# Kernel optimization log

Hardware: AMD Instinct MI355X
Metric: run time of the kernel (lower is better)

The kernel has to match this reference:

```python
import jax, jax.numpy as jnp
import numpy as np

B, N, E, FIN, H, D = 256, 1024, 8192, 8, 4, 5
HD = H * D            # GATv2: 4 heads * 5 dim, concat -> 20
OBS = N               # flattened obs length
AOUT = 64             # action_space_output_dim (aggregator output)
HID = 256             # hidden_size
NOUT = 64             # num_outputs (logits)
NEG = 0.2             # GATv2 leaky_relu negative slope
EPS = 1e-5            # batchnorm eps


def setup_inputs() -> dict:
    key = jax.random.key(0)
    ks = jax.random.split(key, 16)
    def lin(k, i, o):
        return (jax.random.normal(k, (i, o), jnp.float32) / np.sqrt(i)).astype(jnp.float32)
    return {
        "x": jax.random.normal(ks[0], (B, N, FIN), jnp.float32),
        "obs": jax.random.normal(ks[1], (B, OBS), jnp.float32),
        "edge_index": jax.random.randint(ks[2], (2, E), 0, N),
        # GATv2 layer 0 (in=FIN) and layer 1 (in=HD)
        "Wl0": lin(ks[3], FIN, HD), "Wr0": lin(ks[4], FIN, HD),
        "att0": (jax.random.normal(ks[5], (H, D), jnp.float32) * 0.1), "b0": jnp.zeros((HD,), jnp.float32),
        "Wl1": lin(ks[6], HD, HD), "Wr1": lin(ks[7], HD, HD),
        "att1": (jax.random.normal(ks[8], (H, D), jnp.float32) * 0.1), "b1": jnp.zeros((HD,), jnp.float32),
        # BatchNorm params per layer (over feature dim)
        "g0": jnp.ones((HD,), jnp.float32), "be0": jnp.zeros((HD,), jnp.float32),
        "g1": jnp.ones((HD,), jnp.float32), "be1": jnp.zeros((HD,), jnp.float32),
        # aggregator linear (mean pool -> action-space dim)
        "Wagg": lin(ks[9], HD, AOUT), "bagg": jnp.zeros((AOUT,), jnp.float32),
        # logits MLP: cat(agg, obs) -> HID -> HID//2 -> NOUT (tanh activations)
        "W1": lin(ks[10], AOUT + OBS, HID), "bh1": jnp.zeros((HID,), jnp.float32),
        "W2": lin(ks[11], HID, HID // 2), "bh2": jnp.zeros((HID // 2,), jnp.float32),
        "Wout": lin(ks[12], HID // 2, NOUT), "bout": jnp.zeros((NOUT,), jnp.float32),
    }


def _gatv2_single(x, src, dst, Wl, Wr, att, bias):
    # x: [N, Fin]; src/dst: [Es] (with self loops)
    xl = (x @ Wl).reshape(N, H, D)
    xr = (x @ Wr).reshape(N, H, D)
    m = jax.nn.leaky_relu(xl[src] + xr[dst], NEG)        # [Es, H, D]
    e = jnp.einsum('ehd,hd->eh', m, att)                 # [Es, H]
    emax = jax.ops.segment_max(e, dst, num_segments=N)   # every node has a self loop
    p = jnp.exp(e - emax[dst])
    s = jax.ops.segment_sum(p, dst, num_segments=N)
    alpha = p / s[dst]                                   # softmax over incoming edges
    out = jax.ops.segment_sum(alpha[:, :, None] * xl[src], dst, num_segments=N)
    return out.reshape(N, HD) + bias


def _bn(x, g, b):
    # training-mode batchnorm over all (batch, node) positions, per feature
    mu = x.mean(axis=(0, 1))
    var = x.var(axis=(0, 1))
    return (x - mu) * jax.lax.rsqrt(var + EPS) * g + b


def reference(x, obs, edge_index, Wl0, Wr0, att0, b0, Wl1, Wr1, att1, b1,
              g0, be0, g1, be1, Wagg, bagg, W1, bh1, W2, bh2, Wout, bout):
    loops = jnp.arange(N)
    src = jnp.concatenate([edge_index[0], loops])
    dst = jnp.concatenate([edge_index[1], loops])
    layer = lambda xb, Wl, Wr, att, bias: jax.vmap(
        lambda xn: _gatv2_single(xn, src, dst, Wl, Wr, att, bias))(xb)
    h = layer(x, Wl0, Wr0, att0, b0)       # [B, N, HD]
    h = _bn(h, g0, be0)
    h = layer(h, Wl1, Wr1, att1, b1)
    h = _bn(h, g1, be1)
    agg = h.mean(axis=1) @ Wagg + bagg     # mean graph pooling -> [B, AOUT]
    f = jnp.concatenate([agg, obs], axis=1)
    f = jnp.tanh(f @ W1 + bh1)
    f = jnp.tanh(f @ W2 + bh2)
    return f @ Wout + bout                 # logits [B, NOUT]
```

## Files before the change

kernel.cpp:

```cpp
#include <hip/hip_runtime.h>
#include <hip/hip_bf16.h>
#include <math.h>

typedef unsigned short u16;
typedef __attribute__((ext_vector_type(8))) short short8;
typedef __attribute__((ext_vector_type(4))) float floatx4;

constexpr int kN   = 1024;
constexpr int kB   = 256;
constexpr int kE   = 8192;
constexpr int kHD  = 20;
constexpr float kEps = 1e-5f;

static __device__ __forceinline__ float u16_bf16_to_f32(u16 v) {
  return __uint_as_float(((unsigned)v) << 16);
}
static __device__ __forceinline__ void unpack2(unsigned u, float& a, float& b) {
  a = __uint_as_float(u << 16);
  b = __uint_as_float(u & 0xffff0000u);
}
static __device__ __forceinline__ u16 f2bf(float f) {
  __hip_bfloat16 h = __float2bfloat16(f);
  return *reinterpret_cast<u16*>(&h);
}
static __device__ __forceinline__ unsigned pack_bf16(float a, float b) {
  return (unsigned)f2bf(a) | ((unsigned)f2bf(b) << 16);
}

static __device__ __forceinline__ int detect_flag(const unsigned* __restrict__ x) {
  __shared__ int sflag;
  int t = threadIdx.x;
  if (t < 64) {
    unsigned w = x[t];
    unsigned e = (w >> 7) & 0xFFu;
    unsigned long long bl = __ballot(e >= 114u && e <= 136u);
    if (t == 0) sflag = (__popcll(bl) >= 32) ? 1 : 0;
  }
  __syncthreads();
  return sflag;
}

static __device__ __forceinline__ size_t gidx(int n, int b) {
  return ((size_t)(b >> 6) * kN + n) * 64 + (b & 63);
}

struct SmallConv {
  const void* src[17];
  float* dst[17];
  int n[17];
};

struct PrepArgs {
  const unsigned* x;
  const int* ei;
  const void* W1; const void* W2; const void* Wout;
  SmallConv sc;
  u16* xb;
  u16* W1p; u16* W2p; u16* Woutp;
  int* csr_off; int* csr_src;
  float* sums;
};

static __device__ __forceinline__ void repack_one(const void* src, u16* dst, int c, int N, int srcbf) {
  int n = c % N;
  int t2 = c / N;
  int q = t2 & 3, kb = t2 >> 2;
  int k0 = kb * 32 + q * 8;
  u16 w[8];
  if (srcbf) {
    const u16* s = (const u16*)src;
#pragma unroll
    for (int j = 0; j < 8; j++) w[j] = s[(size_t)(k0 + j) * N + n];
  } else {
    const float* s = (const float*)src;
#pragma unroll
    for (int j = 0; j < 8; j++) w[j] = f2bf(s[(size_t)(k0 + j) * N + n]);
  }
  uint4 out;
  out.x = (unsigned)w[0] | ((unsigned)w[1] << 16);
  out.y = (unsigned)w[2] | ((unsigned)w[3] << 16);
  out.z = (unsigned)w[4] | ((unsigned)w[5] << 16);
  out.w = (unsigned)w[6] | ((unsigned)w[7] << 16);
  *((uint4*)(dst + (size_t)c * 8)) = out;
}

__global__ __launch_bounds__(256) void prep_kernel(PrepArgs pa) {
  int bid = blockIdx.x;
  int t = threadIdx.x;
  if (bid == 0) {
    __shared__ int cnt[kN];
    __shared__ int cur[kN];
    __shared__ int wsum[4];
    for (int i = t; i < kN; i += 256) cnt[i] = 0;
    __syncthreads();
    for (int e = t; e < kE; e += 256) atomicAdd(&cnt[pa.ei[kE + e]], 1);
    __syncthreads();
    int d[4], pre[4];
    int s = 0;
#pragma unroll
    for (int j = 0; j < 4; j++) { d[j] = cnt[t * 4 + j] + 1; pre[j] = s; s += d[j]; }
    int lane = t & 63;
    int v = s;
    for (int o = 1; o < 64; o <<= 1) { int u = __shfl_up(v, o); if (lane >= o) v += u; }
    if (lane == 63) wsum[t >> 6] = v;
    __syncthreads();
    int wbase = 0;
    for (int w = 0; w < (t >> 6); w++) wbase += wsum[w];
    int base = wbase + v - s;
#pragma unroll
    for (int j = 0; j < 4; j++) {
      pa.csr_off[t * 4 + j] = base + pre[j];
      cur[t * 4 + j] = base + pre[j];
    }
    if (t == 255) pa.csr_off[kN] = wbase + v;
    __syncthreads();
    for (int e = t; e < kE; e += 256) {
      int sv = pa.ei[e], dv = pa.ei[kE + e];
      int pos = atomicAdd(&cur[dv], 1);
      pa.csr_src[pos] = sv;
    }
    for (int i = t; i < kN; i += 256) {
      int pos = atomicAdd(&cur[i], 1);
      pa.csr_src[pos] = i;
    }
    return;
  }
  int flag = detect_flag(pa.x);
  if (bid == 1) {
    for (int i = t; i < 640; i += 256) pa.sums[i] = 0.f;
    for (int k = 0; k < 17; k++) {
      int n = pa.sc.n[k];
      float* d = pa.sc.dst[k];
      if (flag) {
        const u16* s = (const u16*)pa.sc.src[k];
        for (int i = t; i < n; i += 256) d[i] = u16_bf16_to_f32(s[i]);
      } else {
        const float* s = (const float*)pa.sc.src[k];
        for (int i = t; i < n; i += 256) d[i] = s[i];
      }
    }
    return;
  }
  if (bid < 158) {
    int c = (bid - 2) * 256 + t;
    if (c < 34816) repack_one(pa.W1, pa.W1p, c, 256, flag);
    else if (c < 34816 + 4096) repack_one(pa.W2, pa.W2p, c - 34816, 128, flag);
    else if (c < 34816 + 4096 + 1024) repack_one(pa.Wout, pa.Woutp, c - 34816 - 4096, 64, flag);
    return;
  }
  int rid = (bid - 158) * 256 + t;
  int b = rid >> 10, n = rid & 1023;
  uint4 o;
  if (flag) {
    o = *((const uint4*)((const u16*)pa.x + (size_t)rid * 8));
  } else {
    const float4* s = (const float4*)((const float*)pa.x + (size_t)rid * 8);
    float4 r0 = s[0], r1 = s[1];
    o.x = pack_bf16(r0.x, r0.y); o.y = pack_bf16(r0.z, r0.w);
    o.z = pack_bf16(r1.x, r1.y); o.w = pack_bf16(r1.z, r1.w);
  }
  *((uint4*)(pa.xb + ((size_t)n * kB + b) * 8)) = o;
}

__global__ __launch_bounds__(256) void lin0_kernel(const u16* __restrict__ xb,
                                                   const float* __restrict__ Wl,
                                                   u16* __restrict__ xlb) {
  __shared__ float wl[160];
  int t = threadIdx.x;
  if (t < 160) wl[t] = Wl[t];
  __syncthreads();
  int n = blockIdx.x, b = t;
  uint4 r = *((const uint4*)(xb + ((size_t)n * kB + b) * 8));
  float xi[8];
  unpack2(r.x, xi[0], xi[1]); unpack2(r.y, xi[2], xi[3]);
  unpack2(r.z, xi[4], xi[5]); unpack2(r.w, xi[6], xi[7]);
  float ol[kHD];
#pragma unroll
  for (int f = 0; f < kHD; f++) {
    float al = 0.f;
#pragma unroll
    for (int i = 0; i < 8; i++) al = fmaf(xi[i], wl[i * kHD + f], al);
    ol[f] = al;
  }
  uint2* pl = (uint2*)(xlb + gidx(n, b) * kHD);
#pragma unroll
  for (int k = 0; k < 5; k++)
    pl[k] = make_uint2(pack_bf16(ol[4 * k], ol[4 * k + 1]), pack_bf16(ol[4 * k + 2], ol[4 * k + 3]));
}

__global__ __launch_bounds__(256) void lin1_kernel(const u16* __restrict__ hb,
                                                   const float* __restrict__ sums0,
                                                   const float* __restrict__ g0,
                                                   const float* __restrict__ be0,
                                                   const float* __restrict__ Wl1,
                                                   u16* __restrict__ xlb) {
  __shared__ float wl[400], sbl[kHD], afold[kHD], cfold[kHD], tot[2 * kHD];
  int t = threadIdx.x;
  if (t < 2 * kHD) {
    float v = 0.f;
    for (int k = 0; k < 8; k++) v += sums0[k * 2 * kHD + t];
    tot[t] = v;
  }
  __syncthreads();
  if (t < kHD) {
    const float inv = 1.0f / (float)(kN * kB);
    float mu = tot[t] * inv;
    float var = tot[kHD + t] * inv - mu * mu;
    float a = g0[t] * rsqrtf(var + kEps);
    afold[t] = a;
    cfold[t] = be0[t] - mu * a;
  }
  __syncthreads();
  for (int idx = t; idx < 400; idx += 256) wl[idx] = afold[idx / kHD] * Wl1[idx];
  if (t < kHD) {
    float s = 0.f;
    for (int f = 0; f < kHD; f++) s += cfold[f] * Wl1[f * kHD + t];
    sbl[t] = s;
  }
  __syncthreads();
  int n = blockIdx.x, b = t;
  float hv[kHD];
  {
    const uint2* p = (const uint2*)(hb + gidx(n, b) * kHD);
#pragma unroll
    for (int k = 0; k < 5; k++) {
      uint2 v = p[k];
      unpack2(v.x, hv[4 * k], hv[4 * k + 1]);
      unpack2(v.y, hv[4 * k + 2], hv[4 * k + 3]);
    }
  }
  float ol[kHD];
#pragma unroll
  for (int j = 0; j < kHD; j++) {
    float al = sbl[j];
#pragma unroll
    for (int f = 0; f < kHD; f++) al = fmaf(hv[f], wl[f * kHD + j], al);
    ol[j] = al;
  }
  uint2* pl = (uint2*)(xlb + gidx(n, b) * kHD);
#pragma unroll
  for (int k = 0; k < 5; k++)
    pl[k] = make_uint2(pack_bf16(ol[4 * k], ol[4 * k + 1]), pack_bf16(ol[4 * k + 2], ol[4 * k + 3]));
}

__global__ __launch_bounds__(64) void attn0_kernel(const u16* __restrict__ xlb,
                                                   const u16* __restrict__ xb,
                                                   const float* __restrict__ Wr0,
                                                   const float* __restrict__ att,
                                                   const float* __restrict__ bias,
                                                   const int* __restrict__ csr_off,
                                                   const int* __restrict__ csr_src,
                                                   u16* __restrict__ hout,
                                                   float* __restrict__ sums) {
  __shared__ float satt[kHD], sbias[kHD], swr[160];
  __shared__ int ssrc[128];
  __shared__ float red[2 * kHD];
  int t = threadIdx.x;
  int tb = blockIdx.x & 3;
  int n = blockIdx.x >> 2;
  if (t < kHD) { satt[t] = att[t]; sbias[t] = bias[t]; }
  for (int i = t; i < 160; i += 64) swr[i] = Wr0[i];
  int beg = csr_off[n], end = csr_off[n + 1];
  int deg = end - beg;
  for (int i = t; i < deg && i < 128; i += 64) ssrc[i] = csr_src[beg + i];
  __syncthreads();
  int b = (tb << 6) | t;
  float xrv[kHD];
  {
    uint4 r = *((const uint4*)(xb + ((size_t)n * kB + b) * 8));
    float xi[8];
    unpack2(r.x, xi[0], xi[1]); unpack2(r.y, xi[2], xi[3]);
    unpack2(r.z, xi[4], xi[5]); unpack2(r.w, xi[6], xi[7]);
#pragma unroll
    for (int f = 0; f < kHD; f++) {
      float a = 0.f;
#pragma unroll
      for (int i = 0; i < 8; i++) a = fmaf(xi[i], swr[i * kHD + f], a);
      xrv[f] = a;
    }
  }
  float s[4] = {0.f, 0.f, 0.f, 0.f};
  float acc[kHD];
#pragma unroll
  for (int f = 0; f < kHD; f++) acc[f] = 0.f;

  const size_t tilebase = (size_t)tb * kN * 64 * kHD;
  auto loadrow = [&](int i, uint2 (&rr)[5]) {
    int srcn = (i < 128) ? ssrc[i] : csr_src[beg + i];
    const uint2* p = (const uint2*)(xlb + tilebase + ((size_t)srcn * 64 + t) * kHD);
#pragma unroll
    for (int k = 0; k < 5; k++) rr[k] = p[k];
  };
  auto consume = [&](uint2 (&rr)[5]) {
    float xs[kHD];
#pragma unroll
    for (int k = 0; k < 5; k++) {
      unpack2(rr[k].x, xs[4 * k], xs[4 * k + 1]);
      unpack2(rr[k].y, xs[4 * k + 2], xs[4 * k + 3]);
    }
#pragma unroll
    for (int hh = 0; hh < 4; hh++) {
      float e = 0.f;
#pragma unroll
      for (int d2 = 0; d2 < 5; d2++) {
        int f = hh * 5 + d2;
        float v = xs[f] + xrv[f];
        v = fmaxf(v, 0.2f * v);
        e = fmaf(v, satt[f], e);
      }
      float p = __expf(e);
      s[hh] += p;
#pragma unroll
      for (int d2 = 0; d2 < 5; d2++) {
        int f = hh * 5 + d2;
        acc[f] = fmaf(p, xs[f], acc[f]);
      }
    }
  };

  uint2 r0[5], r1[5];
  loadrow(0, r0);
  if (deg > 1) loadrow(1, r1);
  int i = 0;
  for (; i + 1 < deg; i += 2) {
    consume(r0);
    if (i + 2 < deg) loadrow(i + 2, r0);
    consume(r1);
    if (i + 3 < deg) loadrow(i + 3, r1);
  }
  if (i < deg) consume(r0);

  float hv[kHD];
#pragma unroll
  for (int hh = 0; hh < 4; hh++) {
    float inv = 1.f / s[hh];
#pragma unroll
    for (int d2 = 0; d2 < 5; d2++) {
      int f = hh * 5 + d2;
      hv[f] = fmaf(acc[f], inv, sbias[f]);
    }
  }
  {
    uint2* ph = (uint2*)(hout + tilebase + ((size_t)n * 64 + t) * kHD);
#pragma unroll
    for (int k = 0; k < 5; k++)
      ph[k] = make_uint2(pack_bf16(hv[4 * k], hv[4 * k + 1]), pack_bf16(hv[4 * k + 2], hv[4 * k + 3]));
  }
#pragma unroll
  for (int f = 0; f < kHD; f++) {
    float a = hv[f], q = hv[f] * hv[f];
    for (int o = 32; o > 0; o >>= 1) { a += __shfl_down(a, o); q += __shfl_down(q, o); }
    if (t == 0) { red[f] = a; red[kHD + f] = q; }
  }
  __syncthreads();
  if (t < 2 * kHD) atomicAdd(&sums[(blockIdx.x & 7) * 2 * kHD + t], red[t]);
}

__global__ __launch_bounds__(64) void attn1_kernel(const u16* __restrict__ xlb,
                                                   const u16* __restrict__ hb,
                                                   const float* __restrict__ sums0,
                                                   const float* __restrict__ g0,
                                                   const float* __restrict__ be0,
                                                   const float* __restrict__ Wr1,
                                                   const float* __restrict__ att,
                                                   const float* __restrict__ bias,
                                                   const int* __restrict__ csr_off,
                                                   const int* __restrict__ csr_src,
                                                   u16* __restrict__ hout) {
  __shared__ float satt[kHD], sbias[kHD], swr[400], sbr[kHD];
  __shared__ float afold[kHD], cfold[kHD], tot[2 * kHD];
  __shared__ int ssrc[128];
  int t = threadIdx.x;
  int tb = blockIdx.x & 3;
  int n = blockIdx.x >> 2;
  if (t < kHD) { satt[t] = att[t]; sbias[t] = bias[t]; }
  if (t < 2 * kHD) {
    float v = 0.f;
    for (int k = 0; k < 8; k++) v += sums0[k * 2 * kHD + t];
    tot[t] = v;
  }
  int beg = csr_off[n], end = csr_off[n + 1];
  int deg = end - beg;
  for (int i = t; i < deg && i < 128; i += 64) ssrc[i] = csr_src[beg + i];
  __syncthreads();
  if (t < kHD) {
    const float inv = 1.0f / (float)(kN * kB);
    float mu = tot[t] * inv;
    float var = tot[kHD + t] * inv - mu * mu;
    float a = g0[t] * rsqrtf(var + kEps);
    afold[t] = a;
    cfold[t] = be0[t] - mu * a;
  }
  __syncthreads();
  for (int idx = t; idx < 400; idx += 64) swr[idx] = afold[idx / kHD] * Wr1[idx];
  if (t < kHD) {
    float sv = 0.f;
    for (int f = 0; f < kHD; f++) sv = fmaf(cfold[f], Wr1[f * kHD + t], sv);
    sbr[t] = sv;
  }
  __syncthreads();
  const size_t tilebase = (size_t)tb * kN * 64 * kHD;
  float xrv[kHD];
  {
    float hv0[kHD];
    const uint2* p = (const uint2*)(hb + tilebase + ((size_t)n * 64 + t) * kHD);
#pragma unroll
    for (int k = 0; k < 5; k++) {
      uint2 v = p[k];
      unpack2(v.x, hv0[4 * k], hv0[4 * k + 1]);
      unpack2(v.y, hv0[4 * k + 2], hv0[4 * k + 3]);
    }
#pragma unroll
    for (int j = 0; j < kHD; j++) {
      float a = sbr[j];
#pragma unroll
      for (int f = 0; f < kHD; f++) a = fmaf(hv0[f], swr[f * kHD + j], a);
      xrv[j] = a;
    }
  }
  float s[4] = {0.f, 0.f, 0.f, 0.f};
  float acc[kHD];
#pragma unroll
  for (int f = 0; f < kHD; f++) acc[f] = 0.f;

  auto loadrow = [&](int i, uint2 (&rr)[5]) {
    int srcn = (i < 128) ? ssrc[i] : csr_src[beg + i];
    const uint2* p = (const uint2*)(xlb + tilebase + ((size_t)srcn * 64 + t) * kHD);
#pragma unroll
    for (int k = 0; k < 5; k++) rr[k] = p[k];
  };
  auto consume = [&](uint2 (&rr)[5]) {
    float xs[kHD];
#pragma unroll
    for (int k = 0; k < 5; k++) {
      unpack2(rr[k].x, xs[4 * k], xs[4 * k + 1]);
      unpack2(rr[k].y, xs[4 * k + 2], xs[4 * k + 3]);
    }
#pragma unroll
    for (int hh = 0; hh < 4; hh++) {
      float e = 0.f;
#pragma unroll
      for (int d2 = 0; d2 < 5; d2++) {
        int f = hh * 5 + d2;
        float v = xs[f] + xrv[f];
        v = fmaxf(v, 0.2f * v);
        e = fmaf(v, satt[f], e);
      }
      float p = __expf(e);
      s[hh] += p;
#pragma unroll
      for (int d2 = 0; d2 < 5; d2++) {
        int f = hh * 5 + d2;
        acc[f] = fmaf(p, xs[f], acc[f]);
      }
    }
  };

  uint2 r0[5], r1[5];
  loadrow(0, r0);
  if (deg > 1) loadrow(1, r1);
  int i = 0;
  for (; i + 1 < deg; i += 2) {
    consume(r0);
    if (i + 2 < deg) loadrow(i + 2, r0);
    consume(r1);
    if (i + 3 < deg) loadrow(i + 3, r1);
  }
  if (i < deg) consume(r0);

  float hv[kHD];
#pragma unroll
  for (int hh = 0; hh < 4; hh++) {
    float inv = 1.f / s[hh];
#pragma unroll
    for (int d2 = 0; d2 < 5; d2++) {
      int f = hh * 5 + d2;
      hv[f] = fmaf(acc[f], inv, sbias[f]);
    }
  }
  uint2* ph = (uint2*)(hout + tilebase + ((size_t)n * 64 + t) * kHD);
#pragma unroll
  for (int k = 0; k < 5; k++)
    ph[k] = make_uint2(pack_bf16(hv[4 * k], hv[4 * k + 1]), pack_bf16(hv[4 * k + 2], hv[4 * k + 3]));
}

__global__ __launch_bounds__(64) void pool_kernel(const u16* __restrict__ hb2,
                                                  float* __restrict__ pool_part,
                                                  float* __restrict__ sums1) {
  __shared__ float red[2 * kHD];
  int t = threadIdx.x;
  int tb = blockIdx.x & 3;
  int ch = blockIdx.x >> 2;
  const size_t tilebase = (size_t)tb * kN * 64 * kHD;
  float acc[kHD], q[kHD];
#pragma unroll
  for (int f = 0; f < kHD; f++) { acc[f] = 0.f; q[f] = 0.f; }
  for (int j = 0; j < 64; j++) {
    int n = ch * 64 + j;
    const uint2* p = (const uint2*)(hb2 + tilebase + ((size_t)n * 64 + t) * kHD);
#pragma unroll
    for (int k = 0; k < 5; k++) {
      uint2 v = p[k];
      float a0, a1, a2, a3;
      unpack2(v.x, a0, a1); unpack2(v.y, a2, a3);
      acc[4 * k] += a0;     q[4 * k] += a0 * a0;
      acc[4 * k + 1] += a1; q[4 * k + 1] += a1 * a1;
      acc[4 * k + 2] += a2; q[4 * k + 2] += a2 * a2;
      acc[4 * k + 3] += a3; q[4 * k + 3] += a3 * a3;
    }
  }
  int b = tb * 64 + t;
  float4* pp = (float4*)(pool_part + ((size_t)ch * kB + b) * kHD);
#pragma unroll
  for (int k = 0; k < 5; k++)
    pp[k] = make_float4(acc[4 * k], acc[4 * k + 1], acc[4 * k + 2], acc[4 * k + 3]);
#pragma unroll
  for (int f = 0; f < kHD; f++) {
    float a = acc[f], qq = q[f];
    for (int o = 32; o > 0; o >>= 1) { a += __shfl_down(a, o); qq += __shfl_down(qq, o); }
    if (t == 0) { red[f] = a; red[kHD + f] = qq; }
  }
  __syncthreads();
  if (t < 2 * kHD) atomicAdd(&sums1[(blockIdx.x & 7) * 2 * kHD + t], red[t]);
}

__global__ __launch_bounds__(256) void mlp_kernel(const float* __restrict__ pool_part,
                                                  const float* __restrict__ sums1,
                                                  const float* __restrict__ g1,
                                                  const float* __restrict__ be1,
                                                  const float* __restrict__ Wagg,
                                                  const float* __restrict__ bagg,
                                                  const void* __restrict__ obsraw,
                                                  const u16* __restrict__ W1p,
                                                  const u16* __restrict__ W2p,
                                                  const u16* __restrict__ Woutp,
                                                  const float* __restrict__ bh1,
                                                  const float* __restrict__ bh2,
                                                  const float* __restrict__ bout,
                                                  const unsigned* __restrict__ xdet,
                                                  void* __restrict__ outv) {
  __shared__ __align__(16) u16 fins[16][1096];
  __shared__ __align__(16) u16 h1s[16][264];
  __shared__ __align__(16) u16 h2s[16][136];
  __shared__ float sWagg[1280], pv[16][kHD], a1[kHD], c1[kHD], tot[2 * kHD];
  int flag = detect_flag(xdet);
  int t = threadIdx.x;
  int m0 = blockIdx.x * 16;
  if (t < 2 * kHD) {
    float v = 0.f;
    for (int k = 0; k < 8; k++) v += sums1[k * 2 * kHD + t];
    tot[t] = v;
  }
  for (int idx = t; idx < 1280; idx += 256) sWagg[idx] = Wagg[idx];
  __syncthreads();
  if (t < kHD) {
    const float inv = 1.0f / (float)(kN * kB);
    float mu = tot[t] * inv;
    float var = tot[kHD + t] * inv - mu * mu;
    float a = g1[t] * rsqrtf(var + kEps);
    a1[t] = a;
    c1[t] = be1[t] - mu * a;
  }
  __syncthreads();
  for (int idx = t; idx < 16 * kHD; idx += 256) {
    int bl = idx / kHD, f = idx % kHD;
    float p = 0.f;
    for (int ch = 0; ch < 16; ch++) p += pool_part[((size_t)ch * kB + m0 + bl) * kHD + f];
    pv[bl][f] = (p * (1.0f / kN)) * a1[f] + c1[f];
  }
  for (int idx = t * 8; idx < 16 * 1024; idx += 2048) {
    int r = idx >> 10, c = idx & 1023;
    uint4 o;
    if (flag) {
      o = *((const uint4*)((const u16*)obsraw + (size_t)(m0 + r) * 1024 + c));
    } else {
      const float4* sp = (const float4*)((const float*)obsraw + (size_t)(m0 + r) * 1024 + c);
      float4 r0 = sp[0], r1 = sp[1];
      o.x = pack_bf16(r0.x, r0.y); o.y = pack_bf16(r0.z, r0.w);
      o.z = pack_bf16(r1.x, r1.y); o.w = pack_bf16(r1.z, r1.w);
    }
    *(uint4*)&fins[r][64 + c] = o;
  }
  __syncthreads();
  {
    int j = t & 63, rg = t >> 6;
    for (int r = rg; r < 16; r += 4) {
      float a = bagg[j];
#pragma unroll
      for (int f = 0; f < kHD; f++) a = fmaf(pv[r][f], sWagg[f * 64 + j], a);
      fins[r][j] = f2bf(a);
    }
  }
  __syncthreads();
  int wave = t >> 6, lane = t & 63, lo = lane & 15, quad = lane >> 4;
  {
    floatx4 acc[4] = {{0.f, 0.f, 0.f, 0.f}, {0.f, 0.f, 0.f, 0.f}, {0.f, 0.f, 0.f, 0.f}, {0.f, 0.f, 0.f, 0.f}};
    for (int kb = 0; kb < 34; kb++) {
      short8 a = *(const short8*)&fins[lo][kb * 32 + quad * 8];
#pragma unroll
      for (int nt = 0; nt < 4; nt++) {
        int n0 = (wave * 4 + nt) * 16;
        short8 bf = *(const short8*)(W1p + ((size_t)(kb * 4 + quad) * 256 + n0 + lo) * 8);
        acc[nt] = __builtin_amdgcn_mfma_f32_16x16x32_bf16(a, bf, acc[nt], 0, 0, 0);
      }
    }
#pragma unroll
    for (int nt = 0; nt < 4; nt++) {
      int n0 = (wave * 4 + nt) * 16;
      float bias = bh1[n0 + lo];
#pragma unroll
      for (int r = 0; r < 4; r++) h1s[quad * 4 + r][n0 + lo] = f2bf(tanhf(acc[nt][r] + bias));
    }
  }
  __syncthreads();
  {
    floatx4 acc[2] = {{0.f, 0.f, 0.f, 0.f}, {0.f, 0.f, 0.f, 0.f}};
    for (int kb = 0; kb < 8; kb++) {
      short8 a = *(const short8*)&h1s[lo][kb * 32 + quad * 8];
#pragma unroll
      for (int nt = 0; nt < 2; nt++) {
        int n0 = (wave * 2 + nt) * 16;
        short8 bf = *(const short8*)(W2p + ((size_t)(kb * 4 + quad) * 128 + n0 + lo) * 8);
        acc[nt] = __builtin_amdgcn_mfma_f32_16x16x32_bf16(a, bf, acc[nt], 0, 0, 0);
      }
    }
#pragma unroll
    for (int nt = 0; nt < 2; nt++) {
      int n0 = (wave * 2 + nt) * 16;
      float bias = bh2[n0 + lo];
#pragma unroll
      for (int r = 0; r < 4; r++) h2s[quad * 4 + r][n0 + lo] = f2bf(tanhf(acc[nt][r] + bias));
    }
  }
  __syncthreads();
  {
    int n0 = wave * 16;
    floatx4 acc = {0.f, 0.f, 0.f, 0.f};
    for (int kb = 0; kb < 4; kb++) {
      short8 a = *(const short8*)&h2s[lo][kb * 32 + quad * 8];
      short8 bf = *(const short8*)(Woutp + ((size_t)(kb * 4 + quad) * 64 + n0 + lo) * 8);
      acc = __builtin_amdgcn_mfma_f32_16x16x32_bf16(a, bf, acc, 0, 0, 0);
    }
    float bias = bout[n0 + lo];
    if (flag) {
      __hip_bfloat16* o = (__hip_bfloat16*)outv;
#pragma unroll
      for (int r = 0; r < 4; r++)
        o[(size_t)(m0 + quad * 4 + r) * 64 + n0 + lo] = __float2bfloat16(acc[r] + bias);
    } else {
      float* o = (float*)outv;
#pragma unroll
      for (int r = 0; r < 4; r++)
        o[(size_t)(m0 + quad * 4 + r) * 64 + n0 + lo] = acc[r] + bias;
    }
  }
}

extern "C" void kernel_launch(void* const* d_in, const int* in_sizes, int n_in,
                              void* d_out, int out_size, void* d_ws, size_t ws_size,
                              hipStream_t stream) {
  const int* ei = (const int*)d_in[2];
  char* ws = (char*)d_ws;

  float* sums0     = (float*)(ws + 0);
  float* sums1     = (float*)(ws + 1280);
  int*   csr_off   = (int*)(ws + 2816);
  int*   csr_src   = (int*)(ws + 7168);
  float* convf     = (float*)(ws + 44288);
  u16*   W1p       = (u16*)(ws + 56832);
  u16*   W2p       = (u16*)(ws + 613888);
  u16*   Woutp     = (u16*)(ws + 679424);
  float* pool_part = (float*)(ws + 695808);
  u16*   xb        = (u16*)(ws + 1023744);
  u16*   xlb       = (u16*)(ws + 5218048);
  u16*   hb        = (u16*)(ws + 15703808);
  u16*   hb2       = (u16*)(ws + 26189568);

  const int s_din[17] = {3, 4, 5, 6, 7, 8, 9, 10, 11, 12, 13, 14, 15, 16, 18, 20, 22};
  const int s_n[17]   = {160, 160, 20, 20, 400, 400, 20, 20, 20, 20, 20, 20, 1280, 64, 256, 128, 64};
  SmallConv sc;
  float* fptr[17];
  {
    size_t co = 0;
    for (int i = 0; i < 17; i++) {
      sc.src[i] = d_in[s_din[i]];
      sc.dst[i] = convf + co;
      sc.n[i] = s_n[i];
      fptr[i] = convf + co;
      co += (size_t)s_n[i];
    }
  }
  float* Wl0_f = fptr[0],  *Wr0_f = fptr[1],  *att0_f = fptr[2], *b0_f = fptr[3];
  float* Wl1_f = fptr[4],  *Wr1_f = fptr[5],  *att1_f = fptr[6], *b1_f = fptr[7];
  float* g0_f = fptr[8],   *be0_f = fptr[9],  *g1_f = fptr[10],  *be1_f = fptr[11];
  float* Wagg_f = fptr[12], *bagg_f = fptr[13], *bh1_f = fptr[14], *bh2_f = fptr[15];
  float* bout_f = fptr[16];

  PrepArgs pa;
  pa.x = (const unsigned*)d_in[0];
  pa.ei = ei;
  pa.W1 = d_in[17]; pa.W2 = d_in[19]; pa.Wout = d_in[21];
  pa.sc = sc;
  pa.xb = xb;
  pa.W1p = W1p; pa.W2p = W2p; pa.Woutp = Woutp;
  pa.csr_off = csr_off; pa.csr_src = csr_src;
  pa.sums = sums0;

  prep_kernel<<<1182, 256, 0, stream>>>(pa);
  lin0_kernel<<<kN, 256, 0, stream>>>(xb, Wl0_f, xlb);
  attn0_kernel<<<4 * kN, 64, 0, stream>>>(xlb, xb, Wr0_f, att0_f, b0_f, csr_off, csr_src, hb, sums0);
  lin1_kernel<<<kN, 256, 0, stream>>>(hb, sums0, g0_f, be0_f, Wl1_f, xlb);
  attn1_kernel<<<4 * kN, 64, 0, stream>>>(xlb, hb, sums0, g0_f, be0_f, Wr1_f, att1_f, b1_f,
                                          csr_off, csr_src, hb2);
  pool_kernel<<<64, 64, 0, stream>>>(hb2, pool_part, sums1);
  mlp_kernel<<<16, 256, 0, stream>>>(pool_part, sums1, g1_f, be1_f, Wagg_f, bagg_f, d_in[1],
                                     W1p, W2p, Woutp, bh1_f, bh2_f, bout_f,
                                     (const unsigned*)d_in[0], d_out);
}
```

Baseline: 260.5 us.

## Fuse each GATv2 layer into one per-graph block with LDS-resident features

New measurement: 493.2 us. 1.89x slower.

```diff
diff --git a/kernel.cpp b/kernel.cpp
--- a/kernel.cpp
+++ b/kernel.cpp
@@ -40,10 +40,6 @@
   return sflag;
 }
 
-static __device__ __forceinline__ size_t gidx(int n, int b) {
-  return ((size_t)(b >> 6) * kN + n) * 64 + (b & 63);
-}
-
 struct SmallConv {
   const void* src[17];
   float* dst[17];
@@ -55,7 +51,6 @@
   const int* ei;
   const void* W1; const void* W2; const void* Wout;
   SmallConv sc;
-  u16* xb;
   u16* W1p; u16* W2p; u16* Woutp;
   int* csr_off; int* csr_src;
   float* sums;
@@ -141,66 +136,149 @@
     }
     return;
   }
-  if (bid < 158) {
-    int c = (bid - 2) * 256 + t;
-    if (c < 34816) repack_one(pa.W1, pa.W1p, c, 256, flag);
-    else if (c < 34816 + 4096) repack_one(pa.W2, pa.W2p, c - 34816, 128, flag);
-    else if (c < 34816 + 4096 + 1024) repack_one(pa.Wout, pa.Woutp, c - 34816 - 4096, 64, flag);
-    return;
-  }
-  int rid = (bid - 158) * 256 + t;
-  int b = rid >> 10, n = rid & 1023;
-  uint4 o;
+  int c = (bid - 2) * 256 + t;
+  if (c < 34816) repack_one(pa.W1, pa.W1p, c, 256, flag);
+  else if (c < 34816 + 4096) repack_one(pa.W2, pa.W2p, c - 34816, 128, flag);
+  else if (c < 34816 + 4096 + 1024) repack_one(pa.Wout, pa.Woutp, c - 34816 - 4096, 64, flag);
+}
+
+__global__ __launch_bounds__(1024) void gnn0_kernel(const unsigned* __restrict__ xraw,
+                                                    const float* __restrict__ Wl0,
+                                                    const float* __restrict__ Wr0,
+                                                    const float* __restrict__ att0,
+                                                    const float* __restrict__ b0,
+                                                    const int* __restrict__ csr_off,
+                                                    const int* __restrict__ csr_src,
+                                                    u16* __restrict__ h,
+                                                    float* __restrict__ sums0) {
+  __shared__ u16 sxl[kN * kHD];
+  __shared__ float swl[160], swr[160], satt[kHD], sbias[kHD];
+  __shared__ float red[16][2 * kHD];
+  int flag = detect_flag(xraw);
+  int t = threadIdx.x, b = blockIdx.x;
+  if (t < 160) { swl[t] = Wl0[t]; swr[t] = Wr0[t]; }
+  else if (t >= 256 && t < 256 + kHD) satt[t - 256] = att0[t - 256];
+  else if (t >= 512 && t < 512 + kHD) sbias[t - 512] = b0[t - 512];
+  __syncthreads();
+  float xi[8];
   if (flag) {
-    o = *((const uint4*)((const u16*)pa.x + (size_t)rid * 8));
+    uint4 r = *((const uint4*)((const u16*)xraw + ((size_t)b * kN + t) * 8));
+    unpack2(r.x, xi[0], xi[1]); unpack2(r.y, xi[2], xi[3]);
+    unpack2(r.z, xi[4], xi[5]); unpack2(r.w, xi[6], xi[7]);
   } else {
-    const float4* s = (const float4*)((const float*)pa.x + (size_t)rid * 8);
-    float4 r0 = s[0], r1 = s[1];
-    o.x = pack_bf16(r0.x, r0.y); o.y = pack_bf16(r0.z, r0.w);
-    o.z = pack_bf16(r1.x, r1.y); o.w = pack_bf16(r1.z, r1.w);
-  }
-  *((uint4*)(pa.xb + ((size_t)n * kB + b) * 8)) = o;
-}
-
-__global__ __launch_bounds__(256) void lin0_kernel(const u16* __restrict__ xb,
-                                                   const float* __restrict__ Wl,
-                                                   u16* __restrict__ xlb) {
-  __shared__ float wl[160];
-  int t = threadIdx.x;
-  if (t < 160) wl[t] = Wl[t];
-  __syncthreads();
-  int n = blockIdx.x, b = t;
-  uint4 r = *((const uint4*)(xb + ((size_t)n * kB + b) * 8));
-  float xi[8];
-  unpack2(r.x, xi[0], xi[1]); unpack2(r.y, xi[2], xi[3]);
-  unpack2(r.z, xi[4], xi[5]); unpack2(r.w, xi[6], xi[7]);
-  float ol[kHD];
+    const float4* s4 = (const float4*)((const float*)xraw + ((size_t)b * kN + t) * 8);
+    float4 r0 = s4[0], r1 = s4[1];
+    xi[0] = r0.x; xi[1] = r0.y; xi[2] = r0.z; xi[3] = r0.w;
+    xi[4] = r1.x; xi[5] = r1.y; xi[6] = r1.z; xi[7] = r1.w;
+  }
+  float xrv[kHD];
+  {
+    float ol[kHD];
+#pragma unroll
+    for (int f = 0; f < kHD; f++) {
+      float al = 0.f, ar = 0.f;
+#pragma unroll
+      for (int i = 0; i < 8; i++) {
+        al = fmaf(xi[i], swl[i * kHD + f], al);
+        ar = fmaf(xi[i], swr[i * kHD + f], ar);
+      }
+      ol[f] = al; xrv[f] = ar;
+    }
+    uint2* row = (uint2*)(sxl + t * kHD);
+#pragma unroll
+    for (int k = 0; k < 5; k++)
+      row[k] = make_uint2(pack_bf16(ol[4 * k], ol[4 * k + 1]), pack_bf16(ol[4 * k + 2], ol[4 * k + 3]));
+  }
+  __syncthreads();
+  int beg = csr_off[t], end = csr_off[t + 1];
+  float s[4] = {0.f, 0.f, 0.f, 0.f};
+  float acc[kHD];
+#pragma unroll
+  for (int f = 0; f < kHD; f++) acc[f] = 0.f;
+  for (int idx = beg; idx < end; idx++) {
+    int src = csr_src[idx];
+    const uint2* p = (const uint2*)(sxl + src * kHD);
+    float xs[kHD];
+#pragma unroll
+    for (int k = 0; k < 5; k++) {
+      uint2 v = p[k];
+      unpack2(v.x, xs[4 * k], xs[4 * k + 1]);
+      unpack2(v.y, xs[4 * k + 2], xs[4 * k + 3]);
+    }
+#pragma unroll
+    for (int hh = 0; hh < 4; hh++) {
+      float e = 0.f;
+#pragma unroll
+      for (int d2 = 0; d2 < 5; d2++) {
+        int f = hh * 5 + d2;
+        float v = xs[f] + xrv[f];
+        v = fmaxf(v, 0.2f * v);
+        e = fmaf(v, satt[f], e);
+      }
+      float p2 = __expf(e);
+      s[hh] += p2;
+#pragma unroll
+      for (int d2 = 0; d2 < 5; d2++) {
+        int f = hh * 5 + d2;
+        acc[f] = fmaf(p2, xs[f], acc[f]);
+      }
+    }
+  }
+  float hv[kHD];
+#pragma unroll
+  for (int hh = 0; hh < 4; hh++) {
+    float inv = 1.f / s[hh];
+#pragma unroll
+    for (int d2 = 0; d2 < 5; d2++) {
+      int f = hh * 5 + d2;
+      hv[f] = fmaf(acc[f], inv, sbias[f]);
+    }
+  }
+  {
+    uint2* ph = (uint2*)(h + ((size_t)b * kN + t) * kHD);
+#pragma unroll
+    for (int k = 0; k < 5; k++)
+      ph[k] = make_uint2(pack_bf16(hv[4 * k], hv[4 * k + 1]), pack_bf16(hv[4 * k + 2], hv[4 * k + 3]));
+  }
+  int lane = t & 63, wv = t >> 6;
 #pragma unroll
   for (int f = 0; f < kHD; f++) {
-    float al = 0.f;
-#pragma unroll
-    for (int i = 0; i < 8; i++) al = fmaf(xi[i], wl[i * kHD + f], al);
-    ol[f] = al;
-  }
-  uint2* pl = (uint2*)(xlb + gidx(n, b) * kHD);
-#pragma unroll
-  for (int k = 0; k < 5; k++)
-    pl[k] = make_uint2(pack_bf16(ol[4 * k], ol[4 * k + 1]), pack_bf16(ol[4 * k + 2], ol[4 * k + 3]));
-}
-
-__global__ __launch_bounds__(256) void lin1_kernel(const u16* __restrict__ hb,
-                                                   const float* __restrict__ sums0,
-                                                   const float* __restrict__ g0,
-                                                   const float* __restrict__ be0,
-                                                   const float* __restrict__ Wl1,
-                                                   u16* __restrict__ xlb) {
-  __shared__ float wl[400], sbl[kHD], afold[kHD], cfold[kHD], tot[2 * kHD];
-  int t = threadIdx.x;
+    float a = hv[f], q = hv[f] * hv[f];
+    for (int o = 32; o > 0; o >>= 1) { a += __shfl_down(a, o); q += __shfl_down(q, o); }
+    if (lane == 0) { red[wv][f] = a; red[wv][kHD + f] = q; }
+  }
+  __syncthreads();
+  if (t < 2 * kHD) {
+    float v = 0.f;
+#pragma unroll
+    for (int w = 0; w < 16; w++) v += red[w][t];
+    atomicAdd(&sums0[(b & 7) * 2 * kHD + t], v);
+  }
+}
+
+__global__ __launch_bounds__(1024) void gnn1_kernel(const u16* __restrict__ h,
+                                                    const float* __restrict__ sums0,
+                                                    const float* __restrict__ g0,
+                                                    const float* __restrict__ be0,
+                                                    const float* __restrict__ Wl1,
+                                                    const float* __restrict__ Wr1,
+                                                    const float* __restrict__ att1,
+                                                    const float* __restrict__ b1,
+                                                    const int* __restrict__ csr_off,
+                                                    const int* __restrict__ csr_src,
+                                                    float* __restrict__ pooled,
+                                                    float* __restrict__ sums1) {
+  __shared__ u16 sxl[kN * kHD];
+  __shared__ float swl[400], swr[400], sbl[kHD], sbr[kHD], satt[kHD], sbias[kHD];
+  __shared__ float afold[kHD], cfold[kHD], tot[2 * kHD];
+  __shared__ float red[16][2 * kHD];
+  int t = threadIdx.x, b = blockIdx.x;
   if (t < 2 * kHD) {
     float v = 0.f;
     for (int k = 0; k < 8; k++) v += sums0[k * 2 * kHD + t];
     tot[t] = v;
-  }
+  } else if (t >= 64 && t < 64 + kHD) satt[t - 64] = att1[t - 64];
+  else if (t >= 128 && t < 128 + kHD) sbias[t - 128] = b1[t - 128];
   __syncthreads();
   if (t < kHD) {
     const float inv = 1.0f / (float)(kN * kB);
@@ -211,92 +289,60 @@
     cfold[t] = be0[t] - mu * a;
   }
   __syncthreads();
-  for (int idx = t; idx < 400; idx += 256) wl[idx] = afold[idx / kHD] * Wl1[idx];
-  if (t < kHD) {
-    float s = 0.f;
-    for (int f = 0; f < kHD; f++) s += cfold[f] * Wl1[f * kHD + t];
-    sbl[t] = s;
-  }
-  __syncthreads();
-  int n = blockIdx.x, b = t;
-  float hv[kHD];
-  {
-    const uint2* p = (const uint2*)(hb + gidx(n, b) * kHD);
+  if (t < 400) { swl[t] = afold[t / kHD] * Wl1[t]; swr[t] = afold[t / kHD] * Wr1[t]; }
+  else if (t >= 512 && t < 512 + kHD) {
+    int j = t - 512;
+    float sl = 0.f, sr = 0.f;
+    for (int f = 0; f < kHD; f++) {
+      sl = fmaf(cfold[f], Wl1[f * kHD + j], sl);
+      sr = fmaf(cfold[f], Wr1[f * kHD + j], sr);
+    }
+    sbl[j] = sl; sbr[j] = sr;
+  }
+  __syncthreads();
+  float hv0[kHD];
+  {
+    const uint2* p = (const uint2*)(h + ((size_t)b * kN + t) * kHD);
 #pragma unroll
     for (int k = 0; k < 5; k++) {
       uint2 v = p[k];
-      unpack2(v.x, hv[4 * k], hv[4 * k + 1]);
-      unpack2(v.y, hv[4 * k + 2], hv[4 * k + 3]);
-    }
-  }
-  float ol[kHD];
-#pragma unroll
-  for (int j = 0; j < kHD; j++) {
-    float al = sbl[j];
-#pragma unroll
-    for (int f = 0; f < kHD; f++) al = fmaf(hv[f], wl[f * kHD + j], al);
-    ol[j] = al;
-  }
-  uint2* pl = (uint2*)(xlb + gidx(n, b) * kHD);
-#pragma unroll
-  for (int k = 0; k < 5; k++)
-    pl[k] = make_uint2(pack_bf16(ol[4 * k], ol[4 * k + 1]), pack_bf16(ol[4 * k + 2], ol[4 * k + 3]));
-}
-
-__global__ __launch_bounds__(64) void attn0_kernel(const u16* __restrict__ xlb,
-                                                   const u16* __restrict__ xb,
-                                                   const float* __restrict__ Wr0,
-                                                   const float* __restrict__ att,
-                                                   const float* __restrict__ bias,
-                                                   const int* __restrict__ csr_off,
-                                                   const int* __restrict__ csr_src,
-                                                   u16* __restrict__ hout,
-                                                   float* __restrict__ sums) {
-  __shared__ float satt[kHD], sbias[kHD], swr[160];
-  __shared__ int ssrc[128];
-  __shared__ float red[2 * kHD];
-  int t = threadIdx.x;
-  int tb = blockIdx.x & 3;
-  int n = blockIdx.x >> 2;
-  if (t < kHD) { satt[t] = att[t]; sbias[t] = bias[t]; }
-  for (int i = t; i < 160; i += 64) swr[i] = Wr0[i];
-  int beg = csr_off[n], end = csr_off[n + 1];
-  int deg = end - beg;
-  for (int i = t; i < deg && i < 128; i += 64) ssrc[i] = csr_src[beg + i];
-  __syncthreads();
-  int b = (tb << 6) | t;
+      unpack2(v.x, hv0[4 * k], hv0[4 * k + 1]);
+      unpack2(v.y, hv0[4 * k + 2], hv0[4 * k + 3]);
+    }
+  }
   float xrv[kHD];
   {
-    uint4 r = *((const uint4*)(xb + ((size_t)n * kB + b) * 8));
-    float xi[8];
-    unpack2(r.x, xi[0], xi[1]); unpack2(r.y, xi[2], xi[3]);
-    unpack2(r.z, xi[4], xi[5]); unpack2(r.w, xi[6], xi[7]);
-#pragma unroll
-    for (int f = 0; f < kHD; f++) {
-      float a = 0.f;
-#pragma unroll
-      for (int i = 0; i < 8; i++) a = fmaf(xi[i], swr[i * kHD + f], a);
-      xrv[f] = a;
-    }
-  }
+    float ol[kHD];
+#pragma unroll
+    for (int j = 0; j < kHD; j++) {
+      float al = sbl[j], ar = sbr[j];
+#pragma unroll
+      for (int f = 0; f < kHD; f++) {
+        al = fmaf(hv0[f], swl[f * kHD + j], al);
+        ar = fmaf(hv0[f], swr[f * kHD + j], ar);
+      }
+      ol[j] = al; xrv[j] = ar;
+    }
+    uint2* row = (uint2*)(sxl + t * kHD);
+#pragma unroll
+    for (int k = 0; k < 5; k++)
+      row[k] = make_uint2(pack_bf16(ol[4 * k], ol[4 * k + 1]), pack_bf16(ol[4 * k + 2], ol[4 * k + 3]));
+  }
+  __syncthreads();
+  int beg = csr_off[t], end = csr_off[t + 1];
   float s[4] = {0.f, 0.f, 0.f, 0.f};
   float acc[kHD];
 #pragma unroll
   for (int f = 0; f < kHD; f++) acc[f] = 0.f;
-
-  const size_t tilebase = (size_t)tb * kN * 64 * kHD;
-  auto loadrow = [&](int i, uint2 (&rr)[5]) {
-    int srcn = (i < 128) ? ssrc[i] : csr_src[beg + i];
-    const uint2* p = (const uint2*)(xlb + tilebase + ((size_t)srcn * 64 + t) * kHD);
-#pragma unroll
-    for (int k = 0; k < 5; k++) rr[k] = p[k];
-  };
-  auto consume = [&](uint2 (&rr)[5]) {
+  for (int idx = beg; idx < end; idx++) {
+    int src = csr_src[idx];
+    const uint2* p = (const uint2*)(sxl + src * kHD);
     float xs[kHD];
 #pragma unroll
     for (int k = 0; k < 5; k++) {
-      unpack2(rr[k].x, xs[4 * k], xs[4 * k + 1]);
-      unpack2(rr[k].y, xs[4 * k + 2], xs[4 * k + 3]);
+      uint2 v = p[k];
+      unpack2(v.x, xs[4 * k], xs[4 * k + 1]);
+      unpack2(v.y, xs[4 * k + 2], xs[4 * k + 3]);
     }
 #pragma unroll
     for (int hh = 0; hh < 4; hh++) {
@@ -308,28 +354,15 @@
         v = fmaxf(v, 0.2f * v);
         e = fmaf(v, satt[f], e);
       }
-      float p = __expf(e);
-      s[hh] += p;
+      float p2 = __expf(e);
+      s[hh] += p2;
 #pragma unroll
       for (int d2 = 0; d2 < 5; d2++) {
         int f = hh * 5 + d2;
-        acc[f] = fmaf(p, xs[f], acc[f]);
-      }
-    }
-  };
-
-  uint2 r0[5], r1[5];
-  loadrow(0, r0);
-  if (deg > 1) loadrow(1, r1);
-  int i = 0;
-  for (; i + 1 < deg; i += 2) {
-    consume(r0);
-    if (i + 2 < deg) loadrow(i + 2, r0);
-    consume(r1);
-    if (i + 3 < deg) loadrow(i + 3, r1);
-  }
-  if (i < deg) consume(r0);
-
+        acc[f] = fmaf(p2, xs[f], acc[f]);
+      }
+    }
+  }
   float hv[kHD];
 #pragma unroll
   for (int hh = 0; hh < 4; hh++) {
@@ -340,191 +373,24 @@
       hv[f] = fmaf(acc[f], inv, sbias[f]);
     }
   }
-  {
-    uint2* ph = (uint2*)(hout + tilebase + ((size_t)n * 64 + t) * kHD);
-#pragma unroll
-    for (int k = 0; k < 5; k++)
-      ph[k] = make_uint2(pack_bf16(hv[4 * k], hv[4 * k + 1]), pack_bf16(hv[4 * k + 2], hv[4 * k + 3]));
-  }
+  int lane = t & 63, wv = t >> 6;
 #pragma unroll
   for (int f = 0; f < kHD; f++) {
     float a = hv[f], q = hv[f] * hv[f];
     for (int o = 32; o > 0; o >>= 1) { a += __shfl_down(a, o); q += __shfl_down(q, o); }
-    if (t == 0) { red[f] = a; red[kHD + f] = q; }
-  }
-  __syncthreads();
-  if (t < 2 * kHD) atomicAdd(&sums[(blockIdx.x & 7) * 2 * kHD + t], red[t]);
-}
-
-__global__ __launch_bounds__(64) void attn1_kernel(const u16* __restrict__ xlb,
-                                                   const u16* __restrict__ hb,
-                                                   const float* __restrict__ sums0,
-                                                   const float* __restrict__ g0,
-                                                   const float* __restrict__ be0,
-                                                   const float* __restrict__ Wr1,
-                                                   const float* __restrict__ att,
-                                                   const float* __restrict__ bias,
-                                                   const int* __restrict__ csr_off,
-                                                   const int* __restrict__ csr_src,
-                                                   u16* __restrict__ hout) {
-  __shared__ float satt[kHD], sbias[kHD], swr[400], sbr[kHD];
-  __shared__ float afold[kHD], cfold[kHD], tot[2 * kHD];
-  __shared__ int ssrc[128];
-  int t = threadIdx.x;
-  int tb = blockIdx.x & 3;
-  int n = blockIdx.x >> 2;
-  if (t < kHD) { satt[t] = att[t]; sbias[t] = bias[t]; }
+    if (lane == 0) { red[wv][f] = a; red[wv][kHD + f] = q; }
+  }
+  __syncthreads();
   if (t < 2 * kHD) {
     float v = 0.f;
-    for (int k = 0; k < 8; k++) v += sums0[k * 2 * kHD + t];
-    tot[t] = v;
-  }
-  int beg = csr_off[n], end = csr_off[n + 1];
-  int deg = end - beg;
-  for (int i = t; i < deg && i < 128; i += 64) ssrc[i] = csr_src[beg + i];
-  __syncthreads();
-  if (t < kHD) {
-    const float inv = 1.0f / (float)(kN * kB);
-    float mu = tot[t] * inv;
-    float var = tot[kHD + t] * inv - mu * mu;
-    float a = g0[t] * rsqrtf(var + kEps);
-    afold[t] = a;
-    cfold[t] = be0[t] - mu * a;
-  }
-  __syncthreads();
-  for (int idx = t; idx < 400; idx += 64) swr[idx] = afold[idx / kHD] * Wr1[idx];
-  if (t < kHD) {
-    float sv = 0.f;
-    for (int f = 0; f < kHD; f++) sv = fmaf(cfold[f], Wr1[f * kHD + t], sv);
-    sbr[t] = sv;
-  }
-  __syncthreads();
-  const size_t tilebase = (size_t)tb * kN * 64 * kHD;
-  float xrv[kHD];
-  {
-    float hv0[kHD];
-    const uint2* p = (const uint2*)(hb + tilebase + ((size_t)n * 64 + t) * kHD);
-#pragma unroll
-    for (int k = 0; k < 5; k++) {
-      uint2 v = p[k];
-      unpack2(v.x, hv0[4 * k], hv0[4 * k + 1]);
-      unpack2(v.y, hv0[4 * k + 2], hv0[4 * k + 3]);
-    }
-#pragma unroll
-    for (int j = 0; j < kHD; j++) {
-      float a = sbr[j];
-#pragma unroll
-      for (int f = 0; f < kHD; f++) a = fmaf(hv0[f], swr[f * kHD + j], a);
-      xrv[j] = a;
-    }
-  }
-  float s[4] = {0.f, 0.f, 0.f, 0.f};
-  float acc[kHD];
-#pragma unroll
-  for (int f = 0; f < kHD; f++) acc[f] = 0.f;
-
-  auto loadrow = [&](int i, uint2 (&rr)[5]) {
-    int srcn = (i < 128) ? ssrc[i] : csr_src[beg + i];
-    const uint2* p = (const uint2*)(xlb + tilebase + ((size_t)srcn * 64 + t) * kHD);
-#pragma unroll
-    for (int k = 0; k < 5; k++) rr[k] = p[k];
-  };
-  auto consume = [&](uint2 (&rr)[5]) {
-    float xs[kHD];
-#pragma unroll
-    for (int k = 0; k < 5; k++) {
-      unpack2(rr[k].x, xs[4 * k], xs[4 * k + 1]);
-      unpack2(rr[k].y, xs[4 * k + 2], xs[4 * k + 3]);
-    }
-#pragma unroll
-    for (int hh = 0; hh < 4; hh++) {
-      float e = 0.f;
-#pragma unroll
-      for (int d2 = 0; d2 < 5; d2++) {
-        int f = hh * 5 + d2;
-        float v = xs[f] + xrv[f];
-        v = fmaxf(v, 0.2f * v);
-        e = fmaf(v, satt[f], e);
-      }
-      float p = __expf(e);
-      s[hh] += p;
-#pragma unroll
-      for (int d2 = 0; d2 < 5; d2++) {
-        int f = hh * 5 + d2;
-        acc[f] = fmaf(p, xs[f], acc[f]);
-      }
-    }
-  };
-
-  uint2 r0[5], r1[5];
-  loadrow(0, r0);
-  if (deg > 1) loadrow(1, r1);
-  int i = 0;
-  for (; i + 1 < deg; i += 2) {
-    consume(r0);
-    if (i + 2 < deg) loadrow(i + 2, r0);
-    consume(r1);
-    if (i + 3 < deg) loadrow(i + 3, r1);
-  }
-  if (i < deg) consume(r0);
-
-  float hv[kHD];
-#pragma unroll
-  for (int hh = 0; hh < 4; hh++) {
-    float inv = 1.f / s[hh];
-#pragma unroll
-    for (int d2 = 0; d2 < 5; d2++) {
-      int f = hh * 5 + d2;
-      hv[f] = fmaf(acc[f], inv, sbias[f]);
-    }
-  }
-  uint2* ph = (uint2*)(hout + tilebase + ((size_t)n * 64 + t) * kHD);
-#pragma unroll
-  for (int k = 0; k < 5; k++)
-    ph[k] = make_uint2(pack_bf16(hv[4 * k], hv[4 * k + 1]), pack_bf16(hv[4 * k + 2], hv[4 * k + 3]));
-}
-
-__global__ __launch_bounds__(64) void pool_kernel(const u16* __restrict__ hb2,
-                                                  float* __restrict__ pool_part,
-                                                  float* __restrict__ sums1) {
-  __shared__ float red[2 * kHD];
-  int t = threadIdx.x;
-  int tb = blockIdx.x & 3;
-  int ch = blockIdx.x >> 2;
-  const size_t tilebase = (size_t)tb * kN * 64 * kHD;
-  float acc[kHD], q[kHD];
-#pragma unroll
-  for (int f = 0; f < kHD; f++) { acc[f] = 0.f; q[f] = 0.f; }
-  for (int j = 0; j < 64; j++) {
-    int n = ch * 64 + j;
-    const uint2* p = (const uint2*)(hb2 + tilebase + ((size_t)n * 64 + t) * kHD);
-#pragma unroll
-    for (int k = 0; k < 5; k++) {
-      uint2 v = p[k];
-      float a0, a1, a2, a3;
-      unpack2(v.x, a0, a1); unpack2(v.y, a2, a3);
-      acc[4 * k] += a0;     q[4 * k] += a0 * a0;
-      acc[4 * k + 1] += a1; q[4 * k + 1] += a1 * a1;
-      acc[4 * k + 2] += a2; q[4 * k + 2] += a2 * a2;
-      acc[4 * k + 3] += a3; q[4 * k + 3] += a3 * a3;
-    }
-  }
-  int b = tb * 64 + t;
-  float4* pp = (float4*)(pool_part + ((size_t)ch * kB + b) * kHD);
-#pragma unroll
-  for (int k = 0; k < 5; k++)
-    pp[k] = make_float4(acc[4 * k], acc[4 * k + 1], acc[4 * k + 2], acc[4 * k + 3]);
-#pragma unroll
-  for (int f = 0; f < kHD; f++) {
-    float a = acc[f], qq = q[f];
-    for (int o = 32; o > 0; o >>= 1) { a += __shfl_down(a, o); qq += __shfl_down(qq, o); }
-    if (t == 0) { red[f] = a; red[kHD + f] = qq; }
-  }
-  __syncthreads();
-  if (t < 2 * kHD) atomicAdd(&sums1[(blockIdx.x & 7) * 2 * kHD + t], red[t]);
-}
-
-__global__ __launch_bounds__(256) void mlp_kernel(const float* __restrict__ pool_part,
+#pragma unroll
+    for (int w = 0; w < 16; w++) v += red[w][t];
+    if (t < kHD) pooled[b * kHD + t] = v * (1.0f / kN);
+    atomicAdd(&sums1[(b & 7) * 2 * kHD + t], v);
+  }
+}
+
+__global__ __launch_bounds__(256) void mlp_kernel(const float* __restrict__ pooled,
                                                   const float* __restrict__ sums1,
                                                   const float* __restrict__ g1,
                                                   const float* __restrict__ be1,
@@ -564,9 +430,7 @@
   __syncthreads();
   for (int idx = t; idx < 16 * kHD; idx += 256) {
     int bl = idx / kHD, f = idx % kHD;
-    float p = 0.f;
-    for (int ch = 0; ch < 16; ch++) p += pool_part[((size_t)ch * kB + m0 + bl) * kHD + f];
-    pv[bl][f] = (p * (1.0f / kN)) * a1[f] + c1[f];
+    pv[bl][f] = pooled[(m0 + bl) * kHD + f] * a1[f] + c1[f];
   }
   for (int idx = t * 8; idx < 16 * 1024; idx += 2048) {
     int r = idx >> 10, c = idx & 1023;
@@ -662,19 +526,16 @@
   const int* ei = (const int*)d_in[2];
   char* ws = (char*)d_ws;
 
-  float* sums0     = (float*)(ws + 0);
-  float* sums1     = (float*)(ws + 1280);
-  int*   csr_off   = (int*)(ws + 2816);
-  int*   csr_src   = (int*)(ws + 7168);
-  float* convf     = (float*)(ws + 44288);
-  u16*   W1p       = (u16*)(ws + 56832);
-  u16*   W2p       = (u16*)(ws + 613888);
-  u16*   Woutp     = (u16*)(ws + 679424);
-  float* pool_part = (float*)(ws + 695808);
-  u16*   xb        = (u16*)(ws + 1023744);
-  u16*   xlb       = (u16*)(ws + 5218048);
-  u16*   hb        = (u16*)(ws + 15703808);
-  u16*   hb2       = (u16*)(ws + 26189568);
+  float* sums0   = (float*)(ws + 0);
+  float* sums1   = (float*)(ws + 1280);
+  int*   csr_off = (int*)(ws + 2816);
+  int*   csr_src = (int*)(ws + 7168);
+  float* convf   = (float*)(ws + 44288);
+  u16*   W1p     = (u16*)(ws + 56832);
+  u16*   W2p     = (u16*)(ws + 613888);
+  u16*   Woutp   = (u16*)(ws + 679424);
+  float* pooled  = (float*)(ws + 695808);
+  u16*   hbuf    = (u16*)(ws + 720896);
 
   const int s_din[17] = {3, 4, 5, 6, 7, 8, 9, 10, 11, 12, 13, 14, 15, 16, 18, 20, 22};
   const int s_n[17]   = {160, 160, 20, 20, 400, 400, 20, 20, 20, 20, 20, 20, 1280, 64, 256, 128, 64};
@@ -695,25 +556,23 @@
   float* g0_f = fptr[8],   *be0_f = fptr[9],  *g1_f = fptr[10],  *be1_f = fptr[11];
   float* Wagg_f = fptr[12], *bagg_f = fptr[13], *bh1_f = fptr[14], *bh2_f = fptr[15];
   float* bout_f = fptr[16];
+  (void)g1_f; (void)be1_f;
 
   PrepArgs pa;
   pa.x = (const unsigned*)d_in[0];
   pa.ei = ei;
   pa.W1 = d_in[17]; pa.W2 = d_in[19]; pa.Wout = d_in[21];
   pa.sc = sc;
-  pa.xb = xb;
   pa.W1p = W1p; pa.W2p = W2p; pa.Woutp = Woutp;
   pa.csr_off = csr_off; pa.csr_src = csr_src;
   pa.sums = sums0;
 
-  prep_kernel<<<1182, 256, 0, stream>>>(pa);
-  lin0_kernel<<<kN, 256, 0, stream>>>(xb, Wl0_f, xlb);
-  attn0_kernel<<<4 * kN, 64, 0, stream>>>(xlb, xb, Wr0_f, att0_f, b0_f, csr_off, csr_src, hb, sums0);
-  lin1_kernel<<<kN, 256, 0, stream>>>(hb, sums0, g0_f, be0_f, Wl1_f, xlb);
-  attn1_kernel<<<4 * kN, 64, 0, stream>>>(xlb, hb, sums0, g0_f, be0_f, Wr1_f, att1_f, b1_f,
-                                          csr_off, csr_src, hb2);
-  pool_kernel<<<64, 64, 0, stream>>>(hb2, pool_part, sums1);
-  mlp_kernel<<<16, 256, 0, stream>>>(pool_part, sums1, g1_f, be1_f, Wagg_f, bagg_f, d_in[1],
+  prep_kernel<<<158, 256, 0, stream>>>(pa);
+  gnn0_kernel<<<kB, 1024, 0, stream>>>((const unsigned*)d_in[0], Wl0_f, Wr0_f, att0_f, b0_f,
+                                       csr_off, csr_src, hbuf, sums0);
+  gnn1_kernel<<<kB, 1024, 0, stream>>>(hbuf, sums0, g0_f, be0_f, Wl1_f, Wr1_f, att1_f, b1_f,
+                                       csr_off, csr_src, pooled, sums1);
+  mlp_kernel<<<16, 256, 0, stream>>>(pooled, sums1, fptr[10], fptr[11], Wagg_f, bagg_f, d_in[1],
                                      W1p, W2p, Woutp, bh1_f, bh2_f, bout_f,
                                      (const unsigned*)d_in[0], d_out);
 }
```
